# Kernel tuning notes

Hardware: AMD Instinct MI355X
Metric: run time of the kernel (lower is better)

Reference implementation:

```python
import jax, jax.numpy as jnp
import numpy as np

D = 1024      # features
C = 768       # context dim
H = 16        # heads
HD = D // H   # head dim = 64
N = 2048      # query tokens
M = 2048      # context tokens
EPS = 1e-12
SCALE = float(np.sqrt(HD))


def layernorm(x, w, b):
    c = x - x.mean(axis=-1, keepdims=True)
    s = (c * c).mean(axis=-1, keepdims=True)
    return c * jax.lax.rsqrt(s + EPS) * w + b


def setup_inputs() -> dict:
    key = jax.random.key(0)
    ks = jax.random.split(key, 10)
    sc = 0.02
    return {
        "x": jax.random.normal(ks[0], (N, D), jnp.float32),
        "ctx": jax.random.normal(ks[1], (M, C), jnp.float32),
        # attention projections (Projection: normal*0.02, zero bias)
        "wq": jax.random.normal(ks[2], (D, D), jnp.float32) * sc,
        "bq": jnp.zeros((D,), jnp.float32),
        "wk": jax.random.normal(ks[3], (C, D), jnp.float32) * sc,
        "bk": jnp.zeros((D,), jnp.float32),
        "wv": jax.random.normal(ks[4], (C, D), jnp.float32) * sc,
        "bv": jnp.zeros((D,), jnp.float32),
        "wo": jax.random.normal(ks[5], (D, D), jnp.float32) * sc,
        "bo": jnp.zeros((D,), jnp.float32),
        # MLP
        "w1": jax.random.normal(ks[6], (D, 4 * D), jnp.float32) * sc,
        "b1": jnp.zeros((4 * D,), jnp.float32),
        "w2": jax.random.normal(ks[7], (4 * D, D), jnp.float32) * sc,
        "b2": jnp.zeros((D,), jnp.float32),
        # layernorms
        "qn_w": jnp.ones((D,), jnp.float32), "qn_b": jnp.zeros((D,), jnp.float32),
        "kvn_w": jnp.ones((C,), jnp.float32), "kvn_b": jnp.zeros((C,), jnp.float32),
        "pn_w": jnp.ones((D,), jnp.float32), "pn_b": jnp.zeros((D,), jnp.float32),
    }


def reference(x, ctx, wq, bq, wk, bk, wv, bv, wo, bo, w1, b1, w2, b2,
              qn_w, qn_b, kvn_w, kvn_b, pn_w, pn_b):
    # pre-norm cross-attention
    xq = layernorm(x, qn_w, qn_b)          # [n, d]
    kv = layernorm(ctx, kvn_w, kvn_b)      # [m, c]
    q = (xq @ wq + bq).reshape(N, H, HD).transpose(1, 0, 2)   # [h, n, hd]
    k = (kv @ wk + bk).reshape(M, H, HD).transpose(1, 0, 2)   # [h, m, hd]
    v = (kv @ wv + bv).reshape(M, H, HD).transpose(1, 0, 2)   # [h, m, hd]
    attn = jax.nn.softmax(jnp.einsum('hnd,hmd->hnm', q, k) / SCALE, axis=-1)
    o = jnp.einsum('hnm,hmd->hnd', attn, v).transpose(1, 0, 2).reshape(N, D)
    x = (o @ wo + bo) + x
    # MLP block
    h = layernorm(x, pn_w, pn_b)
    h = jax.nn.gelu(h @ w1 + b1) @ w2 + b2
    return h + x
```

## Files before the change

kernel.cpp:

```cpp
#include <hip/hip_runtime.h>

typedef __bf16 bf16;
typedef __bf16 bf16x4 __attribute__((ext_vector_type(4)));
typedef __bf16 bf16x8 __attribute__((ext_vector_type(8)));
typedef float f32x4 __attribute__((ext_vector_type(4)));

#define N_TOK 2048
#define M_TOK 2048
#define DIM 1024
#define CDIM 768
#define DFF 4096

static __device__ __forceinline__ void async16(const void* g, void* l) {
  __builtin_amdgcn_global_load_lds((const __attribute__((address_space(1))) void*)g,
                                   (__attribute__((address_space(3))) void*)l, 16, 0, 0);
}

__device__ __forceinline__ bool detect_bf(const void* xprobe, float* sbuf) {
  int* cnt = (int*)sbuf;
  if (threadIdx.x == 0) *cnt = 0;
  __syncthreads();
  const unsigned* w = (const unsigned*)xprobe;
  int ok = 0;
  for (int i = threadIdx.x; i < 512; i += 256) {
    unsigned lo = w[i] & 0xFFFFu;
    float f = __uint_as_float(lo << 16);
    if (lo == 0u || (fabsf(f) > 1e-3f && fabsf(f) < 1e3f)) ok++;
  }
  atomicAdd(cnt, ok);
  __syncthreads();
  return *cnt >= 256;
}

__device__ __forceinline__ void t32(int bx, int by, const void* in, bf16* out,
                                    int r0, int Rcnt, int c0, int Cfull,
                                    bool isbf, bf16* t) {
  const int cb = bx * 32, rb = by * 32;
  const int tx = threadIdx.x & 31, ty = threadIdx.x >> 5;
#pragma unroll
  for (int i = 0; i < 4; i++) {
    const size_t r = (size_t)(r0 + rb + ty + i * 8);
    const size_t c = (size_t)(c0 + cb + tx);
    float v = isbf ? (float)((const bf16*)in)[r * Cfull + c]
                   : ((const float*)in)[r * Cfull + c];
    t[(ty + i * 8) * 33 + tx] = (bf16)v;
  }
  __syncthreads();
#pragma unroll
  for (int i = 0; i < 4; i++)
    out[(size_t)(cb + ty + i * 8) * Rcnt + rb + tx] = t[tx * 33 + ty + i * 8];
}

__device__ __forceinline__ void ln_row(const void* x, const void* wr, const void* br,
                                       bf16* outp, int cols, int row,
                                       bool in_bf, bool w_bf,
                                       float* xrow, float* sh) {
  const bf16* xr_b = (const bf16*)x + (size_t)row * cols;
  const float* xr_f = (const float*)x + (size_t)row * cols;
  bf16* orow = outp + (size_t)row * cols;
  float s = 0.f, ss = 0.f;
  for (int c = threadIdx.x; c < cols; c += 256) {
    float v = in_bf ? (float)xr_b[c] : xr_f[c];
    xrow[c] = v;
    s += v; ss += v * v;
  }
  for (int d = 1; d < 64; d <<= 1) { s += __shfl_xor(s, d, 64); ss += __shfl_xor(ss, d, 64); }
  const int wv = threadIdx.x >> 6, lane = threadIdx.x & 63;
  if (lane == 0) { sh[wv] = s; sh[4 + wv] = ss; }
  __syncthreads();
  s = sh[0] + sh[1] + sh[2] + sh[3];
  ss = sh[4] + sh[5] + sh[6] + sh[7];
  const float mean = s / cols;
  float var = ss / cols - mean * mean;
  var = fmaxf(var, 0.f);
  const float r = rsqrtf(var + 1e-12f);
  for (int c = threadIdx.x; c < cols; c += 256) {
    const float wv2 = w_bf ? (float)((const bf16*)wr)[c] : ((const float*)wr)[c];
    const float bv2 = w_bf ? (float)((const bf16*)br)[c] : ((const float*)br)[c];
    orow[c] = (bf16)((xrow[c] - mean) * r * wv2 + bv2);
  }
}

struct PrepArgs {
  const void* tsrc[4]; bf16* tdst[4]; int tRcnt[4], tCfull[4], tgy[4];
  const void* x; const void* qnw; const void* qnb; bf16* xq;
  const void* ctx; const void* kvnw; const void* kvnb; bf16* kvn;
  const void* csrc[12]; bf16* cdst[12]; int cn[12];
  const void* xprobe;
};
__global__ __launch_bounds__(256) void prep_kernel(PrepArgs a, int* flag) {
  __shared__ __align__(16) float sbuf[1040];
  const int z = blockIdx.z;
  const bool isbf = detect_bf(a.xprobe, sbuf);
  if (z < 4) {
    if ((int)blockIdx.y >= a.tgy[z]) return;
    t32(blockIdx.x, blockIdx.y, a.tsrc[z], a.tdst[z], 0, a.tRcnt[z], 0, a.tCfull[z],
        isbf, (bf16*)sbuf);
  } else if (z < 8) {
    const int row = blockIdx.x + 32 * blockIdx.y + (z & 1) * 1024;
    if (z < 6) ln_row(a.x,   a.qnw,  a.qnb,  a.xq,  DIM,  row, isbf, isbf, sbuf, sbuf + 1024);
    else       ln_row(a.ctx, a.kvnw, a.kvnb, a.kvn, CDIM, row, isbf, isbf, sbuf, sbuf + 1024);
  } else {
    const int b = blockIdx.x + 32 * blockIdx.y;
    if (b == 0 && threadIdx.x == 0) *flag = isbf ? 1 : 0;
    if (b >= 12) return;
    const void* in = a.csrc[b];
    bf16* out = a.cdst[b];
    const int n = a.cn[b];
    for (int i = threadIdx.x; i < n; i += 256)
      out[i] = isbf ? ((const bf16*)in)[i] : (bf16)((const float*)in)[i];
  }
}

struct PostArgs {
  const void* w2; bf16* w2T;
  const bf16* xat; const void* pnw; const void* pnb; bf16* hln;
};
__global__ __launch_bounds__(256) void post_kernel(PostArgs a, const int* flag) {
  __shared__ __align__(16) float sbuf[1040];
  const bool isbf = (*flag != 0);
  if (blockIdx.z == 0) {
    const int tbx = blockIdx.x & 31, tby = blockIdx.y + 32 * (blockIdx.x >> 5);
    t32(tbx, tby, a.w2, a.w2T, 0, 2048, 0, DIM, isbf, (bf16*)sbuf);
  } else {
    const int row = blockIdx.x + 64 * blockIdx.y;
    ln_row(a.xat, a.pnw, a.pnb, a.hln, DIM, row, true, isbf, sbuf, sbuf + 1024);
  }
}

__device__ __forceinline__ float gelu_f(float x) {
  float u = 0.7978845608028654f * (x + 0.044715f * x * x * x);
  return 0.5f * x * (1.f + tanhf(u));
}

template <int EPI>
__device__ __forceinline__ void gemm_body(
    int bx, int by,
    const bf16* __restrict__ A, const bf16* __restrict__ Bt,
    const bf16* __restrict__ bias, const void* __restrict__ resid,
    void* __restrict__ Cout, int K, int ldc, const int* flag) {
  __shared__ __align__(16) bf16 As[2][64 * 64];
  __shared__ __align__(16) bf16 Bs[2][64 * 64];
  const int tid = threadIdx.x;
  const int lane = tid & 63, wv = tid >> 6;
  const int lq = lane >> 4, lm = lane & 15;
  const int row0 = by * 64, col0 = bx * 64;
  const int wr = (wv >> 1) * 32, wc = (wv & 1) * 32;

  const int sr = lane >> 3;
  const int sc = ((lane & 7) ^ sr) * 8;
  const int swz = (lm & 7) << 3;

  f32x4 acc[2][2] = {};

  const bf16* Abase = A + (size_t)(row0 + wv * 16 + sr) * K + sc;
  const bf16* Bbase = Bt + (size_t)(col0 + wv * 16 + sr) * K + sc;

  const int nt = K >> 6;
#pragma unroll
  for (int b = 0; b < 2; b++) {
    async16(Abase + (size_t)(b * 8) * K, &As[0][wv * 1024 + b * 512]);
    async16(Bbase + (size_t)(b * 8) * K, &Bs[0][wv * 1024 + b * 512]);
  }
  __syncthreads();

  int cur = 0;
  for (int t = 0; t < nt; ++t) {
    if (t + 1 < nt) {
      const int k1 = (t + 1) << 6;
#pragma unroll
      for (int b = 0; b < 2; b++) {
        async16(Abase + (size_t)(b * 8) * K + k1, &As[cur ^ 1][wv * 1024 + b * 512]);
        async16(Bbase + (size_t)(b * 8) * K + k1, &Bs[cur ^ 1][wv * 1024 + b * 512]);
      }
    }
#pragma unroll
    for (int kh = 0; kh < 2; kh++) {
      const int cofs = (kh * 32 + lq * 8) ^ swz;
      bf16x8 af[2], bfv[2];
#pragma unroll
      for (int i = 0; i < 2; i++)
        af[i] = *(const bf16x8*)&As[cur][(wr + i * 16 + lm) * 64 + cofs];
#pragma unroll
      for (int j = 0; j < 2; j++)
        bfv[j] = *(const bf16x8*)&Bs[cur][(wc + j * 16 + lm) * 64 + cofs];
#pragma unroll
      for (int i = 0; i < 2; i++)
#pragma unroll
        for (int j = 0; j < 2; j++)
          acc[i][j] = __builtin_amdgcn_mfma_f32_16x16x32_bf16(af[i], bfv[j], acc[i][j], 0, 0, 0);
    }
    __syncthreads();
    cur ^= 1;
  }

  const bool isbf = (*flag != 0);
#pragma unroll
  for (int i = 0; i < 2; i++) {
    const int rb = row0 + wr + i * 16 + lq * 4;
#pragma unroll
    for (int j = 0; j < 2; j++) {
      const int c = col0 + wc + j * 16 + lm;
      const float bv = (EPI != 5) ? (float)bias[c] : 0.f;
#pragma unroll
      for (int rg = 0; rg < 4; rg++) {
        const size_t idx = (size_t)(rb + rg) * ldc + c;
        float v = acc[i][j][rg] + bv;
        if (EPI == 1)
          v += isbf ? (float)((const bf16*)resid)[idx] : ((const float*)resid)[idx];
        if (EPI == 2) v = gelu_f(v);
        if (EPI == 4) v += (float)((const bf16*)resid)[idx];
        if (EPI == 5)
          v += isbf ? (float)((bf16*)Cout)[idx] : ((float*)Cout)[idx];
        if (EPI == 4 || EPI == 5) {
          if (isbf) ((bf16*)Cout)[idx] = (bf16)v;
          else      ((float*)Cout)[idx] = v;
        } else {
          ((bf16*)Cout)[idx] = (bf16)v;
        }
      }
    }
  }
}

template <int EPI>
__global__ __launch_bounds__(256) void gemm64db(
    const bf16* __restrict__ A, const bf16* __restrict__ Bt,
    const bf16* __restrict__ bias, const void* __restrict__ resid,
    void* __restrict__ Cout, int K, int ldc, const int* flag) {
  const int gx = gridDim.x;
  const int nwg = gx * gridDim.y;
  const int fid = blockIdx.x + gx * blockIdx.y;
  const int sid = (fid & 7) * (nwg >> 3) + (fid >> 3);
  gemm_body<EPI>(sid % gx, sid / gx, A, Bt, bias, resid, Cout, K, ldc, flag);
}

struct Mlp2Args {
  const bf16* h1; const bf16* w2T; const bf16* b2; const bf16* xat; void* out;
  const void* w1raw; bf16* w1Tdst;
  const void* w2raw; bf16* w2Tdst;
};
__global__ __launch_bounds__(256) void mlp2h0_fused(Mlp2Args a, const int* flag) {
  const int z = blockIdx.z;
  if (z == 0) {
    if ((int)blockIdx.x >= 16) return;
    const int fid = blockIdx.x + 16 * blockIdx.y;
    const int sid = (fid & 7) * 64 + (fid >> 3);
    gemm_body<4>(sid & 15, sid >> 4, a.h1, a.w2T, a.b2, a.xat, a.out,
                 2048, DIM, flag);
  } else {
    __shared__ __align__(16) bf16 t[32 * 33];
    const bool isbf = (*flag != 0);
    if (z == 1) {
      t32(blockIdx.x, blockIdx.y, a.w1raw, a.w1Tdst, 0, DIM, 2048, DFF, isbf, t);
    } else {
      const int tbx = blockIdx.x & 31, tby = blockIdx.y + 32 * (blockIdx.x >> 5);
      t32(tbx, tby, a.w2raw, a.w2Tdst, 2048, 2048, 0, DIM, isbf, t);
    }
  }
}

struct QkvArgs {
  const bf16* A[3];
  const bf16* Bt[3];
  const bf16* bias[3];
  bf16* C[3];
  int K[3], ldc[3], brow[3];
};
__global__ __launch_bounds__(256) void gemm64db_qkv(QkvArgs a) {
  const int z = blockIdx.z;
  int gx, bx0, by0;
  if (z < 2) { gx = 16; bx0 = blockIdx.y; by0 = blockIdx.x; }
  else       { gx = 32; bx0 = blockIdx.x; by0 = blockIdx.y; }
  const int fid = bx0 + gx * by0;
  const int sid = (fid & 7) * 64 + (fid >> 3);
  const int bx = sid % gx, by = sid / gx;
  const bf16* A = a.A[z];
  const bf16* Bt = a.Bt[z];
  const int K = a.K[z];
  __shared__ __align__(16) bf16 As[2][64 * 64];
  __shared__ __align__(16) bf16 Bs[2][64 * 64];
  const int tid = threadIdx.x;
  const int lane = tid & 63, wv = tid >> 6;
  const int lq = lane >> 4, lm = lane & 15;
  const int row0 = by * 64, col0 = bx * 64;
  const int wr = (wv >> 1) * 32, wc = (wv & 1) * 32;

  const int sr = lane >> 3;
  const int sc = ((lane & 7) ^ sr) * 8;
  const int swz = (lm & 7) << 3;

  f32x4 acc[2][2] = {};

  const bf16* Abase = A + (size_t)(row0 + wv * 16 + sr) * K + sc;
  const bf16* Bbase = Bt + (size_t)(col0 + wv * 16 + sr) * K + sc;

  const int nt = K >> 6;
#pragma unroll
  for (int b = 0; b < 2; b++) {
    async16(Abase + (size_t)(b * 8) * K, &As[0][wv * 1024 + b * 512]);
    async16(Bbase + (size_t)(b * 8) * K, &Bs[0][wv * 1024 + b * 512]);
  }
  __syncthreads();

  int cur = 0;
  for (int t = 0; t < nt; ++t) {
    if (t + 1 < nt) {
      const int k1 = (t + 1) << 6;
#pragma unroll
      for (int b = 0; b < 2; b++) {
        async16(Abase + (size_t)(b * 8) * K + k1, &As[cur ^ 1][wv * 1024 + b * 512]);
        async16(Bbase + (size_t)(b * 8) * K + k1, &Bs[cur ^ 1][wv * 1024 + b * 512]);
      }
    }
#pragma unroll
    for (int kh = 0; kh < 2; kh++) {
      const int cofs = (kh * 32 + lq * 8) ^ swz;
      bf16x8 af[2], bfv[2];
#pragma unroll
      for (int i = 0; i < 2; i++)
        af[i] = *(const bf16x8*)&As[cur][(wr + i * 16 + lm) * 64 + cofs];
#pragma unroll
      for (int j = 0; j < 2; j++)
        bfv[j] = *(const bf16x8*)&Bs[cur][(wc + j * 16 + lm) * 64 + cofs];
#pragma unroll
      for (int i = 0; i < 2; i++)
#pragma unroll
        for (int j = 0; j < 2; j++)
          acc[i][j] = __builtin_amdgcn_mfma_f32_16x16x32_bf16(af[i], bfv[j], acc[i][j], 0, 0, 0);
    }
    __syncthreads();
    cur ^= 1;
  }

  const bf16* bias = a.bias[z];
  bf16* C = a.C[z];
  const int ldc = a.ldc[z];
  const bool brow = a.brow[z] != 0;
#pragma unroll
  for (int i = 0; i < 2; i++) {
    const int rb = row0 + wr + i * 16 + lq * 4;
#pragma unroll
    for (int j = 0; j < 2; j++) {
      const int c = col0 + wc + j * 16 + lm;
      const float bcol = brow ? 0.f : (float)bias[c];
#pragma unroll
      for (int rg = 0; rg < 4; rg++) {
        const float bv = brow ? (float)bias[rb + rg] : bcol;
        C[(size_t)(rb + rg) * ldc + c] = (bf16)(acc[i][j][rg] + bv);
      }
    }
  }
}

__global__ __launch_bounds__(512) void attn_kernel(
    const bf16* __restrict__ q, const bf16* __restrict__ k,
    const bf16* __restrict__ vT, bf16* __restrict__ pO0, bf16* __restrict__ pO1,
    float* __restrict__ l0, float* __restrict__ l1,
    const void* __restrict__ w1raw, bf16* __restrict__ w1Tdst,
    const int* __restrict__ flag) {
  __shared__ __align__(16) bf16 KPs[128 * 128];
  __shared__ __align__(16) bf16 Vs[64 * 128];
  const int z = blockIdx.z;
  if (z >= 2) {
    if (threadIdx.x >= 256) return;
    const int id = blockIdx.x + 16 * blockIdx.y + 256 * (z - 2);
    const bool isbf = (*flag != 0);
    t32(id & 63, id >> 6, w1raw, w1Tdst, 0, DIM, 0, DFF, isbf, (bf16*)KPs);
    return;
  }
  const int tid = threadIdx.x, lane = tid & 63, wv = tid >> 6;
  const int lq = lane >> 4, lm = lane & 15;
  const int fid = blockIdx.x + 16 * (blockIdx.y + 16 * z);
  const int sid = (fid & 7) * 64 + (fid >> 3);
  const int n0 = (sid & 15) * 128;
  const int h = (sid >> 4) & 15;
  const int half = sid >> 8;
  const int mbeg = half * (M_TOK / 2), mend = mbeg + M_TOK / 2;
  bf16* pO = half ? pO1 : pO0;
  float* lb = half ? l1 : l0;

  bf16x8 qf[2];
#pragma unroll
  for (int f = 0; f < 2; f++)
    qf[f] = *(const bf16x8*)&q[(size_t)(n0 + wv * 16 + lm) * DIM + h * 64 + f * 32 + lq * 8];

  f32x4 oacc[4] = {};
  float lsum = 0.f;
  const float sc = 0.125f * 1.4426950408889634f;

  bf16x8 kreg[2], vreg[2];
#pragma unroll
  for (int it = 0; it < 2; it++) {
    const int e = tid * 8 + it * 4096;
    kreg[it] = *(const bf16x8*)&k[(size_t)(mbeg + (e >> 6)) * DIM + h * 64 + (e & 63)];
    vreg[it] = *(const bf16x8*)&vT[(size_t)(h * 64 + (e >> 7)) * M_TOK + mbeg + (e & 127)];
  }

  for (int m0 = mbeg; m0 < mend; m0 += 128) {
    asm volatile("s_waitcnt lgkmcnt(0)" ::: "memory");
    __builtin_amdgcn_s_barrier();
#pragma unroll
    for (int it = 0; it < 2; it++) {
      const int e = tid * 8 + it * 4096;
      const int kr = e >> 6, kc = e & 63;
      *(bf16x8*)&KPs[kr * 64 + (kc ^ ((kr & 7) << 3))] = kreg[it];
      const int vr = e >> 7, vc = e & 127;
      *(bf16x8*)&Vs[vr * 128 + (vc ^ ((vr & 7) << 3))] = vreg[it];
    }
    if (m0 + 128 < mend) {
      const int m1 = m0 + 128;
#pragma unroll
      for (int it = 0; it < 2; it++) {
        const int e = tid * 8 + it * 4096;
        kreg[it] = *(const bf16x8*)&k[(size_t)(m1 + (e >> 6)) * DIM + h * 64 + (e & 63)];
        vreg[it] = *(const bf16x8*)&vT[(size_t)(h * 64 + (e >> 7)) * M_TOK + m1 + (e & 127)];
      }
    }
    asm volatile("s_waitcnt lgkmcnt(0)" ::: "memory");
    __builtin_amdgcn_s_barrier();

    f32x4 s[8];
    __builtin_amdgcn_s_setprio(1);
#pragma unroll
    for (int j = 0; j < 8; j++) {
      const int kswz = (lm & 7) << 3;
      bf16x8 kf0 = *(const bf16x8*)&KPs[(j * 16 + lm) * 64 + ((lq * 8) ^ kswz)];
      bf16x8 kf1 = *(const bf16x8*)&KPs[(j * 16 + lm) * 64 + ((32 + lq * 8) ^ kswz)];
      f32x4 zz = {};
      zz = __builtin_amdgcn_mfma_f32_16x16x32_bf16(kf0, qf[0], zz, 0, 0, 0);
      s[j] = __builtin_amdgcn_mfma_f32_16x16x32_bf16(kf1, qf[1], zz, 0, 0, 0);
    }
    __builtin_amdgcn_s_setprio(0);
    asm volatile("s_waitcnt lgkmcnt(0)" ::: "memory");
    __builtin_amdgcn_s_barrier();

#pragma unroll
    for (int j = 0; j < 8; j++) {
      bf16x4 pw;
#pragma unroll
      for (int rg = 0; rg < 4; rg++) {
        const float pv = exp2f(s[j][rg] * sc);
        lsum += pv;
        pw[rg] = (bf16)pv;
      }
      *(bf16x4*)&KPs[(wv * 16 + lm) * 128 + ((j * 16 + lq * 4) ^ ((lm & 7) << 3))] = pw;
    }

    __builtin_amdgcn_s_setprio(1);
#pragma unroll
    for (int kk = 0; kk < 4; kk++) {
      bf16x8 pf = *(const bf16x8*)&KPs[(wv * 16 + lm) * 128 +
                                       ((kk * 32 + lq * 8) ^ ((lm & 7) << 3))];
#pragma unroll
      for (int dt = 0; dt < 4; dt++) {
        bf16x8 vf = *(const bf16x8*)&Vs[(dt * 16 + lm) * 128 +
                                        ((kk * 32 + lq * 8) ^ ((lm & 7) << 3))];
        oacc[dt] = __builtin_amdgcn_mfma_f32_16x16x32_bf16(vf, pf, oacc[dt], 0, 0, 0);
      }
    }
    __builtin_amdgcn_s_setprio(0);
  }

  lsum += __shfl_xor(lsum, 16, 64);
  lsum += __shfl_xor(lsum, 32, 64);
  if (lane < 16) lb[h * N_TOK + n0 + wv * 16 + lane] = lsum;

  const int rn = n0 + wv * 16 + lm;
#pragma unroll
  for (int dt = 0; dt < 4; dt++) {
    bf16x4 ow;
#pragma unroll
    for (int rg = 0; rg < 4; rg++) ow[rg] = (bf16)oacc[dt][rg];
    *(bf16x4*)&pO[(size_t)rn * DIM + h * 64 + dt * 16 + lq * 4] = ow;
  }
}

__global__ __launch_bounds__(256) void attn_combine(
    const bf16* __restrict__ pO0, const bf16* __restrict__ pO1,
    const float* __restrict__ l0, const float* __restrict__ l1,
    bf16* __restrict__ om) {
  const int i4 = (blockIdx.x * 256 + threadIdx.x) * 4;
  const int n = i4 >> 10;
  const int h = (i4 & 1023) >> 6;
  const float rinv = 1.f / (l0[h * N_TOK + n] + l1[h * N_TOK + n]);
  bf16x4 a = *(const bf16x4*)&pO0[i4];
  bf16x4 b = *(const bf16x4*)&pO1[i4];
  bf16x4 o;
#pragma unroll
  for (int r = 0; r < 4; r++) o[r] = (bf16)(((float)a[r] + (float)b[r]) * rinv);
  *(bf16x4*)&om[i4] = o;
}

extern "C" void kernel_launch(void* const* d_in, const int* in_sizes, int n_in,
                              void* d_out, int out_size, void* d_ws, size_t ws_size,
                              hipStream_t stream) {
  const void* x_r     = d_in[0];
  const void* ctx_r   = d_in[1];
  const void* wq_r    = d_in[2];
  const void* bq_r    = d_in[3];
  const void* wk_r    = d_in[4];
  const void* bk_r    = d_in[5];
  const void* wv_r    = d_in[6];
  const void* bv_r    = d_in[7];
  const void* wo_r    = d_in[8];
  const void* bo_r    = d_in[9];
  const void* w1_r    = d_in[10];
  const void* b1_r    = d_in[11];
  const void* w2_r    = d_in[12];
  const void* b2_r    = d_in[13];
  const void* qnw_r   = d_in[14];
  const void* qnb_r   = d_in[15];
  const void* kvnw_r  = d_in[16];
  const void* kvnb_r  = d_in[17];
  const void* pnw_r   = d_in[18];
  const void* pnb_r   = d_in[19];

  bf16* p = (bf16*)d_ws;
  const size_t MEG = 1024 * 1024;
  bf16* qm  = p;             bf16* hln = qm;
  bf16* km  = p + 2 * MEG;   bf16* xat = km;
  bf16* wC  = p + 4 * MEG;
  bf16* xq  = p + 8 * MEG;   bf16* pO0 = xq;   bf16* om = xq;
  bf16* vTb = p + 10 * MEG;
  bf16* kvn = p + 12 * MEG;  bf16* pO1 = kvn;
  bf16* h1h = p + 10 * MEG;
  bf16* SM  = p + 14 * MEG;
  int* flag = (int*)(p + 14 * MEG + 16384);

  bf16* wqT = wC;
  bf16* wkT = wC + 1 * MEG;
  bf16* wvT = wC + 1 * MEG + 786432;
  bf16* woT = wC + 2 * MEG + 524288;
  bf16* w1Th = wC;
  bf16* w2Th = wC + 2 * MEG;
  bf16* w2Ts = p + 8 * MEG;
  float* l0 = (float*)(wC + 3584 * 1024);
  float* l1 = l0 + N_TOK * 16;

  bf16* bqc = SM, *bkc = SM + 1024, *bvc = SM + 2048, *boc = SM + 3072;
  bf16* b1c = SM + 4096, *b2c = SM + 8192;
  bf16* qnw = SM + 9216, *qnb = SM + 10240;
  bf16* kvnw = SM + 11264, *kvnb = SM + 12032;
  bf16* pnw = SM + 12800, *pnb = SM + 13824;

  {
    PrepArgs pa;
    pa.tsrc[0] = wq_r; pa.tdst[0] = wqT; pa.tRcnt[0] = DIM;  pa.tCfull[0] = DIM; pa.tgy[0] = 32;
    pa.tsrc[1] = wk_r; pa.tdst[1] = wkT; pa.tRcnt[1] = CDIM; pa.tCfull[1] = DIM; pa.tgy[1] = 24;
    pa.tsrc[2] = wv_r; pa.tdst[2] = wvT; pa.tRcnt[2] = CDIM; pa.tCfull[2] = DIM; pa.tgy[2] = 24;
    pa.tsrc[3] = wo_r; pa.tdst[3] = woT; pa.tRcnt[3] = DIM;  pa.tCfull[3] = DIM; pa.tgy[3] = 32;
    pa.x = x_r;   pa.qnw = qnw_r;   pa.qnb = qnb_r;   pa.xq = xq;
    pa.ctx = ctx_r; pa.kvnw = kvnw_r; pa.kvnb = kvnb_r; pa.kvn = kvn;
    pa.csrc[0] = bq_r;   pa.cdst[0] = bqc;  pa.cn[0] = DIM;
    pa.csrc[1] = bk_r;   pa.cdst[1] = bkc;  pa.cn[1] = DIM;
    pa.csrc[2] = bv_r;   pa.cdst[2] = bvc;  pa.cn[2] = DIM;
    pa.csrc[3] = bo_r;   pa.cdst[3] = boc;  pa.cn[3] = DIM;
    pa.csrc[4] = b1_r;   pa.cdst[4] = b1c;  pa.cn[4] = DFF;
    pa.csrc[5] = b2_r;   pa.cdst[5] = b2c;  pa.cn[5] = DIM;
    pa.csrc[6] = qnw_r;  pa.cdst[6] = qnw;  pa.cn[6] = DIM;
    pa.csrc[7] = qnb_r;  pa.cdst[7] = qnb;  pa.cn[7] = DIM;
    pa.csrc[8] = kvnw_r; pa.cdst[8] = kvnw; pa.cn[8] = CDIM;
    pa.csrc[9] = kvnb_r; pa.cdst[9] = kvnb; pa.cn[9] = CDIM;
    pa.csrc[10] = pnw_r; pa.cdst[10] = pnw; pa.cn[10] = DIM;
    pa.csrc[11] = pnb_r; pa.cdst[11] = pnb; pa.cn[11] = DIM;
    pa.xprobe = x_r;
    prep_kernel<<<dim3(32, 32, 9), 256, 0, stream>>>(pa, flag);
  }

  {
    QkvArgs qa;
    qa.A[0] = xq;  qa.Bt[0] = wqT; qa.bias[0] = bqc; qa.C[0] = qm;
    qa.K[0] = DIM;  qa.ldc[0] = DIM;   qa.brow[0] = 0;
    qa.A[1] = kvn; qa.Bt[1] = wkT; qa.bias[1] = bkc; qa.C[1] = km;
    qa.K[1] = CDIM; qa.ldc[1] = DIM;   qa.brow[1] = 0;
    qa.A[2] = wvT; qa.Bt[2] = kvn; qa.bias[2] = bvc; qa.C[2] = vTb;
    qa.K[2] = CDIM; qa.ldc[2] = M_TOK; qa.brow[2] = 1;
    gemm64db_qkv<<<dim3(32, 16, 3), 256, 0, stream>>>(qa);
  }

  attn_kernel<<<dim3(16, 16, 10), 512, 0, stream>>>(qm, km, vTb, pO0, pO1,
                                                    l0, l1, w1_r, w1Th, flag);
  attn_combine<<<2048, 256, 0, stream>>>(pO0, pO1, l0, l1, om);

  gemm64db<1><<<dim3(16, 32), 256, 0, stream>>>(om, woT, boc, x_r, xat, DIM, DIM, flag);

  {
    PostArgs po;
    po.w2 = w2_r; po.w2T = w2Th;
    po.xat = xat; po.pnw = pnw_r; po.pnb = pnb_r; po.hln = hln;
    post_kernel<<<dim3(64, 32, 2), 256, 0, stream>>>(po, flag);
  }

  gemm64db<2><<<dim3(32, 32), 256, 0, stream>>>(hln, w1Th, b1c, nullptr,
                                                h1h, DIM, 2048, flag);

  {
    Mlp2Args ma;
    ma.h1 = h1h; ma.w2T = w2Th; ma.b2 = b2c; ma.xat = xat; ma.out = d_out;
    ma.w1raw = w1_r; ma.w1Tdst = w1Th;
    ma.w2raw = w2_r; ma.w2Tdst = w2Ts;
    mlp2h0_fused<<<dim3(64, 32, 3), 256, 0, stream>>>(ma, flag);
  }

  gemm64db<2><<<dim3(32, 32), 256, 0, stream>>>(hln, w1Th, b1c + 2048, nullptr,
                                                h1h, DIM, 2048, flag);
  gemm64db<5><<<dim3(16, 32), 256, 0, stream>>>(h1h, w2Ts, b2c, nullptr, d_out,
                                                2048, DIM, flag);
}
```

Measured before the change: 333.8 us.

## Use 128-deep K staging for MLP2 GEMMs and async LDS loads in attention

Adds a GEMM body that stages two 64-wide K slices per pipeline step (128 K per barrier pair, 64KB LDS) and uses it for both MLP down-projection halves, halving the number of barriers per tile. Separately, the attention loop replaces register-prefetched K/V tiles stored to LDS with direct global_load_lds async copies using a swizzled layout. The attention change drops the cross-iteration register prefetch, so loads are now issued and waited on within the same iteration, which may expose memory latency. The larger LDS footprint may also lower occupancy for the GEMMs.

```diff
diff --git a/kernel.cpp b/kernel.cpp
--- a/kernel.cpp
+++ b/kernel.cpp
@@ -134,66 +134,9 @@
 }
 
 template <int EPI>
-__device__ __forceinline__ void gemm_body(
-    int bx, int by,
-    const bf16* __restrict__ A, const bf16* __restrict__ Bt,
-    const bf16* __restrict__ bias, const void* __restrict__ resid,
-    void* __restrict__ Cout, int K, int ldc, const int* flag) {
-  __shared__ __align__(16) bf16 As[2][64 * 64];
-  __shared__ __align__(16) bf16 Bs[2][64 * 64];
-  const int tid = threadIdx.x;
-  const int lane = tid & 63, wv = tid >> 6;
-  const int lq = lane >> 4, lm = lane & 15;
-  const int row0 = by * 64, col0 = bx * 64;
-  const int wr = (wv >> 1) * 32, wc = (wv & 1) * 32;
-
-  const int sr = lane >> 3;
-  const int sc = ((lane & 7) ^ sr) * 8;
-  const int swz = (lm & 7) << 3;
-
-  f32x4 acc[2][2] = {};
-
-  const bf16* Abase = A + (size_t)(row0 + wv * 16 + sr) * K + sc;
-  const bf16* Bbase = Bt + (size_t)(col0 + wv * 16 + sr) * K + sc;
-
-  const int nt = K >> 6;
-#pragma unroll
-  for (int b = 0; b < 2; b++) {
-    async16(Abase + (size_t)(b * 8) * K, &As[0][wv * 1024 + b * 512]);
-    async16(Bbase + (size_t)(b * 8) * K, &Bs[0][wv * 1024 + b * 512]);
-  }
-  __syncthreads();
-
-  int cur = 0;
-  for (int t = 0; t < nt; ++t) {
-    if (t + 1 < nt) {
-      const int k1 = (t + 1) << 6;
-#pragma unroll
-      for (int b = 0; b < 2; b++) {
-        async16(Abase + (size_t)(b * 8) * K + k1, &As[cur ^ 1][wv * 1024 + b * 512]);
-        async16(Bbase + (size_t)(b * 8) * K + k1, &Bs[cur ^ 1][wv * 1024 + b * 512]);
-      }
-    }
-#pragma unroll
-    for (int kh = 0; kh < 2; kh++) {
-      const int cofs = (kh * 32 + lq * 8) ^ swz;
-      bf16x8 af[2], bfv[2];
-#pragma unroll
-      for (int i = 0; i < 2; i++)
-        af[i] = *(const bf16x8*)&As[cur][(wr + i * 16 + lm) * 64 + cofs];
-#pragma unroll
-      for (int j = 0; j < 2; j++)
-        bfv[j] = *(const bf16x8*)&Bs[cur][(wc + j * 16 + lm) * 64 + cofs];
-#pragma unroll
-      for (int i = 0; i < 2; i++)
-#pragma unroll
-        for (int j = 0; j < 2; j++)
-          acc[i][j] = __builtin_amdgcn_mfma_f32_16x16x32_bf16(af[i], bfv[j], acc[i][j], 0, 0, 0);
-    }
-    __syncthreads();
-    cur ^= 1;
-  }
-
+__device__ __forceinline__ void gemm_epi(
+    f32x4 (&acc)[2][2], int row0, int col0, int wr, int wc, int lq, int lm,
+    const bf16* bias, const void* resid, void* Cout, int ldc, const int* flag) {
   const bool isbf = (*flag != 0);
 #pragma unroll
   for (int i = 0; i < 2; i++) {
@@ -224,6 +167,141 @@
 }
 
 template <int EPI>
+__device__ __forceinline__ void gemm_body(
+    int bx, int by,
+    const bf16* __restrict__ A, const bf16* __restrict__ Bt,
+    const bf16* __restrict__ bias, const void* __restrict__ resid,
+    void* __restrict__ Cout, int K, int ldc, const int* flag) {
+  __shared__ __align__(16) bf16 As[2][64 * 64];
+  __shared__ __align__(16) bf16 Bs[2][64 * 64];
+  const int tid = threadIdx.x;
+  const int lane = tid & 63, wv = tid >> 6;
+  const int lq = lane >> 4, lm = lane & 15;
+  const int row0 = by * 64, col0 = bx * 64;
+  const int wr = (wv >> 1) * 32, wc = (wv & 1) * 32;
+
+  const int sr = lane >> 3;
+  const int sc = ((lane & 7) ^ sr) * 8;
+  const int swz = (lm & 7) << 3;
+
+  f32x4 acc[2][2] = {};
+
+  const bf16* Abase = A + (size_t)(row0 + wv * 16 + sr) * K + sc;
+  const bf16* Bbase = Bt + (size_t)(col0 + wv * 16 + sr) * K + sc;
+
+  const int nt = K >> 6;
+#pragma unroll
+  for (int b = 0; b < 2; b++) {
+    async16(Abase + (size_t)(b * 8) * K, &As[0][wv * 1024 + b * 512]);
+    async16(Bbase + (size_t)(b * 8) * K, &Bs[0][wv * 1024 + b * 512]);
+  }
+  __syncthreads();
+
+  int cur = 0;
+  for (int t = 0; t < nt; ++t) {
+    if (t + 1 < nt) {
+      const int k1 = (t + 1) << 6;
+#pragma unroll
+      for (int b = 0; b < 2; b++) {
+        async16(Abase + (size_t)(b * 8) * K + k1, &As[cur ^ 1][wv * 1024 + b * 512]);
+        async16(Bbase + (size_t)(b * 8) * K + k1, &Bs[cur ^ 1][wv * 1024 + b * 512]);
+      }
+    }
+#pragma unroll
+    for (int kh = 0; kh < 2; kh++) {
+      const int cofs = (kh * 32 + lq * 8) ^ swz;
+      bf16x8 af[2], bfv[2];
+#pragma unroll
+      for (int i = 0; i < 2; i++)
+        af[i] = *(const bf16x8*)&As[cur][(wr + i * 16 + lm) * 64 + cofs];
+#pragma unroll
+      for (int j = 0; j < 2; j++)
+        bfv[j] = *(const bf16x8*)&Bs[cur][(wc + j * 16 + lm) * 64 + cofs];
+#pragma unroll
+      for (int i = 0; i < 2; i++)
+#pragma unroll
+        for (int j = 0; j < 2; j++)
+          acc[i][j] = __builtin_amdgcn_mfma_f32_16x16x32_bf16(af[i], bfv[j], acc[i][j], 0, 0, 0);
+    }
+    __syncthreads();
+    cur ^= 1;
+  }
+  gemm_epi<EPI>(acc, row0, col0, wr, wc, lq, lm, bias, resid, Cout, ldc, flag);
+}
+
+template <int EPI>
+__device__ __forceinline__ void gemm_body128(
+    int bx, int by,
+    const bf16* __restrict__ A, const bf16* __restrict__ Bt,
+    const bf16* __restrict__ bias, const void* __restrict__ resid,
+    void* __restrict__ Cout, int K, int ldc, const int* flag, bf16* lds) {
+  const int tid = threadIdx.x;
+  const int lane = tid & 63, wv = tid >> 6;
+  const int lq = lane >> 4, lm = lane & 15;
+  const int row0 = by * 64, col0 = bx * 64;
+  const int wr = (wv >> 1) * 32, wc = (wv & 1) * 32;
+
+  const int sr = lane >> 3;
+  const int sc = ((lane & 7) ^ sr) * 8;
+  const int swz = (lm & 7) << 3;
+
+  f32x4 acc[2][2] = {};
+
+  const bf16* Abase = A + (size_t)(row0 + wv * 16 + sr) * K + sc;
+  const bf16* Bbase = Bt + (size_t)(col0 + wv * 16 + sr) * K + sc;
+
+  const int np = K >> 7;
+#pragma unroll
+  for (int s = 0; s < 2; s++)
+#pragma unroll
+    for (int b = 0; b < 2; b++) {
+      async16(Abase + (size_t)(b * 8) * K + s * 64, lds + (s)*4096 + wv * 1024 + b * 512);
+      async16(Bbase + (size_t)(b * 8) * K + s * 64, lds + (2 + s) * 4096 + wv * 1024 + b * 512);
+    }
+  __syncthreads();
+
+  int cur = 0;
+  for (int t = 0; t < np; ++t) {
+    if (t + 1 < np) {
+      const int k1 = (t + 1) << 7;
+      bf16* nb = lds + (cur ^ 1) * 16384;
+#pragma unroll
+      for (int s = 0; s < 2; s++)
+#pragma unroll
+        for (int b = 0; b < 2; b++) {
+          async16(Abase + (size_t)(b * 8) * K + k1 + s * 64, nb + s * 4096 + wv * 1024 + b * 512);
+          async16(Bbase + (size_t)(b * 8) * K + k1 + s * 64, nb + (2 + s) * 4096 + wv * 1024 + b * 512);
+        }
+    }
+    const bf16* cb = lds + cur * 16384;
+#pragma unroll
+    for (int s = 0; s < 2; s++) {
+      const bf16* Asb = cb + s * 4096;
+      const bf16* Bsb = cb + (2 + s) * 4096;
+#pragma unroll
+      for (int kh = 0; kh < 2; kh++) {
+        const int cofs = (kh * 32 + lq * 8) ^ swz;
+        bf16x8 af[2], bfv[2];
+#pragma unroll
+        for (int i = 0; i < 2; i++)
+          af[i] = *(const bf16x8*)&Asb[(wr + i * 16 + lm) * 64 + cofs];
+#pragma unroll
+        for (int j = 0; j < 2; j++)
+          bfv[j] = *(const bf16x8*)&Bsb[(wc + j * 16 + lm) * 64 + cofs];
+#pragma unroll
+        for (int i = 0; i < 2; i++)
+#pragma unroll
+          for (int j = 0; j < 2; j++)
+            acc[i][j] = __builtin_amdgcn_mfma_f32_16x16x32_bf16(af[i], bfv[j], acc[i][j], 0, 0, 0);
+      }
+    }
+    __syncthreads();
+    cur ^= 1;
+  }
+  gemm_epi<EPI>(acc, row0, col0, wr, wc, lq, lm, bias, resid, Cout, ldc, flag);
+}
+
+template <int EPI>
 __global__ __launch_bounds__(256) void gemm64db(
     const bf16* __restrict__ A, const bf16* __restrict__ Bt,
     const bf16* __restrict__ bias, const void* __restrict__ resid,
@@ -235,27 +313,40 @@
   gemm_body<EPI>(sid % gx, sid / gx, A, Bt, bias, resid, Cout, K, ldc, flag);
 }
 
+template <int EPI>
+__global__ __launch_bounds__(256) void gemm64k128(
+    const bf16* __restrict__ A, const bf16* __restrict__ Bt,
+    const bf16* __restrict__ bias, const void* __restrict__ resid,
+    void* __restrict__ Cout, int K, int ldc, const int* flag) {
+  __shared__ __align__(16) bf16 lds[32768];
+  const int gx = gridDim.x;
+  const int nwg = gx * gridDim.y;
+  const int fid = blockIdx.x + gx * blockIdx.y;
+  const int sid = (fid & 7) * (nwg >> 3) + (fid >> 3);
+  gemm_body128<EPI>(sid % gx, sid / gx, A, Bt, bias, resid, Cout, K, ldc, flag, lds);
+}
+
 struct Mlp2Args {
   const bf16* h1; const bf16* w2T; const bf16* b2; const bf16* xat; void* out;
   const void* w1raw; bf16* w1Tdst;
   const void* w2raw; bf16* w2Tdst;
 };
 __global__ __launch_bounds__(256) void mlp2h0_fused(Mlp2Args a, const int* flag) {
+  __shared__ __align__(16) bf16 lds[32768];
   const int z = blockIdx.z;
   if (z == 0) {
     if ((int)blockIdx.x >= 16) return;
     const int fid = blockIdx.x + 16 * blockIdx.y;
     const int sid = (fid & 7) * 64 + (fid >> 3);
-    gemm_body<4>(sid & 15, sid >> 4, a.h1, a.w2T, a.b2, a.xat, a.out,
-                 2048, DIM, flag);
+    gemm_body128<4>(sid & 15, sid >> 4, a.h1, a.w2T, a.b2, a.xat, a.out,
+                    2048, DIM, flag, lds);
   } else {
-    __shared__ __align__(16) bf16 t[32 * 33];
     const bool isbf = (*flag != 0);
     if (z == 1) {
-      t32(blockIdx.x, blockIdx.y, a.w1raw, a.w1Tdst, 0, DIM, 2048, DFF, isbf, t);
+      t32(blockIdx.x, blockIdx.y, a.w1raw, a.w1Tdst, 0, DIM, 2048, DFF, isbf, lds);
     } else {
       const int tbx = blockIdx.x & 31, tby = blockIdx.y + 32 * (blockIdx.x >> 5);
-      t32(tbx, tby, a.w2raw, a.w2Tdst, 2048, 2048, 0, DIM, isbf, t);
+      t32(tbx, tby, a.w2raw, a.w2Tdst, 2048, 2048, 0, DIM, isbf, lds);
     }
   }
 }
@@ -389,36 +480,23 @@
   float lsum = 0.f;
   const float sc = 0.125f * 1.4426950408889634f;
 
-  bf16x8 kreg[2], vreg[2];
-#pragma unroll
-  for (int it = 0; it < 2; it++) {
-    const int e = tid * 8 + it * 4096;
-    kreg[it] = *(const bf16x8*)&k[(size_t)(mbeg + (e >> 6)) * DIM + h * 64 + (e & 63)];
-    vreg[it] = *(const bf16x8*)&vT[(size_t)(h * 64 + (e >> 7)) * M_TOK + mbeg + (e & 127)];
-  }
+  const int l3 = lane >> 3, l4 = lane >> 4;
+  const bf16* kb = k + (size_t)(wv * 16 + l3) * DIM + h * 64 + (((lane & 7) ^ l3) << 3);
+  const bf16* vb0 = vT + (size_t)(h * 64 + wv * 8 + l4) * M_TOK + (((lane & 15) ^ l4) << 3);
+  const bf16* vb1 = vT + (size_t)(h * 64 + wv * 8 + 4 + l4) * M_TOK + (((lane & 15) ^ (4 + l4)) << 3);
+  bf16* kd = KPs + wv * 1024;
+  bf16* vd = Vs + wv * 1024;
 
   for (int m0 = mbeg; m0 < mend; m0 += 128) {
-    asm volatile("s_waitcnt lgkmcnt(0)" ::: "memory");
-    __builtin_amdgcn_s_barrier();
-#pragma unroll
-    for (int it = 0; it < 2; it++) {
-      const int e = tid * 8 + it * 4096;
-      const int kr = e >> 6, kc = e & 63;
-      *(bf16x8*)&KPs[kr * 64 + (kc ^ ((kr & 7) << 3))] = kreg[it];
-      const int vr = e >> 7, vc = e & 127;
-      *(bf16x8*)&Vs[vr * 128 + (vc ^ ((vr & 7) << 3))] = vreg[it];
-    }
-    if (m0 + 128 < mend) {
-      const int m1 = m0 + 128;
-#pragma unroll
-      for (int it = 0; it < 2; it++) {
-        const int e = tid * 8 + it * 4096;
-        kreg[it] = *(const bf16x8*)&k[(size_t)(m1 + (e >> 6)) * DIM + h * 64 + (e & 63)];
-        vreg[it] = *(const bf16x8*)&vT[(size_t)(h * 64 + (e >> 7)) * M_TOK + m1 + (e & 127)];
-      }
-    }
-    asm volatile("s_waitcnt lgkmcnt(0)" ::: "memory");
-    __builtin_amdgcn_s_barrier();
+    __syncthreads();
+    {
+      const bf16* kt = kb + (size_t)m0 * DIM;
+      async16(kt, kd);
+      async16(kt + (size_t)8 * DIM, kd + 512);
+      async16(vb0 + m0, vd);
+      async16(vb1 + m0, vd + 512);
+    }
+    __syncthreads();
 
     f32x4 s[8];
     __builtin_amdgcn_s_setprio(1);
@@ -605,6 +683,6 @@
 
   gemm64db<2><<<dim3(32, 32), 256, 0, stream>>>(hln, w1Th, b1c + 2048, nullptr,
                                                 h1h, DIM, 2048, flag);
-  gemm64db<5><<<dim3(16, 32), 256, 0, stream>>>(h1h, w2Ts, b2c, nullptr, d_out,
-                                                2048, DIM, flag);
-}
+  gemm64k128<5><<<dim3(16, 32), 256, 0, stream>>>(h1h, w2Ts, b2c, nullptr, d_out,
+                                                  2048, DIM, flag);
+}
```

After: 336.9 us. About the same (+0.9%).
